# Kernel tuning notes

Hardware: AMD Instinct MI355X
Metric: run time of the kernel (lower is better)

Reference implementation:

```python
import jax, jax.numpy as jnp
import numpy as np

G = 8          # deformable groups
K = 9          # 3x3 kernel points
MAXR = 10.0    # max_residue_magnitude


def conv2d(x, w, b):
    # x: [B,Cin,H,W], w: [Cout,Cin,3,3], SAME padding, stride 1
    y = jax.lax.conv_general_dilated(x, w, (1, 1), ((1, 1), (1, 1)),
                                     dimension_numbers=('NCHW', 'OIHW', 'NCHW'))
    return y + b[None, :, None, None]


def lrelu(x):
    return jnp.where(x >= 0, x, 0.1 * x)


def offset_branch(x, ws, bs):
    for w, b in zip(ws[:-1], bs[:-1]):
        x = lrelu(conv2d(x, w, b))
    return conv2d(x, ws[-1], bs[-1])


def mdcn(x, offset, mask, w, b):
    # Modulated deformable conv, 3x3, stride 1, pad 1, dilation 1, groups=1.
    # offset: [B, G*K*2, H, W] ordered (g, k, (y,x)); mask: [B, G*K, H, W]
    B, C, H, W = x.shape
    Cg = C // G
    off = offset.reshape(B, G, K, 2, H, W)
    m = mask.reshape(B, G, K, H, W)
    ky = (jnp.arange(K) // 3 - 1).astype(x.dtype)   # kernel dy, pad=1
    kx = (jnp.arange(K) % 3 - 1).astype(x.dtype)    # kernel dx
    hy = jnp.arange(H, dtype=x.dtype)
    wx = jnp.arange(W, dtype=x.dtype)
    py = hy[None, None, None, :, None] + ky[None, None, :, None, None] + off[:, :, :, 0]  # [B,G,K,H,W]
    px = wx[None, None, None, None, :] + kx[None, None, :, None, None] + off[:, :, :, 1]
    y0f = jnp.floor(py); x0f = jnp.floor(px)
    ly = py - y0f; lx = px - x0f
    y0 = y0f.astype(jnp.int32); x0 = x0f.astype(jnp.int32)
    xf = x.reshape(B, G, Cg, H * W)

    def gather(yi, xi):
        valid = ((yi >= 0) & (yi < H) & (xi >= 0) & (xi < W)).astype(x.dtype)
        yc = jnp.clip(yi, 0, H - 1)
        xc = jnp.clip(xi, 0, W - 1)
        idx = (yc * W + xc).reshape(B, G, 1, K * H * W)
        v = jnp.take_along_axis(xf, idx, axis=3).reshape(B, G, Cg, K, H, W)
        return v * valid.reshape(B, G, 1, K, H, W)

    ly_ = ly[:, :, None]; lx_ = lx[:, :, None]  # [B,G,1,K,H,W]
    samp = (gather(y0, x0) * (1 - ly_) * (1 - lx_)
            + gather(y0, x0 + 1) * (1 - ly_) * lx_
            + gather(y0 + 1, x0) * ly_ * (1 - lx_)
            + gather(y0 + 1, x0 + 1) * ly_ * lx_)
    samp = samp * m[:, :, None]                 # modulation
    wr = w.reshape(w.shape[0], G, Cg, K)        # [Cout,G,Cg,K]
    return jnp.einsum('ogck,bgckhw->bohw', wr, samp) + b[None, :, None, None]


def setup_inputs():
    key = jax.random.key(0)
    ks = jax.random.split(key, 40)
    B, C, H, W = 1, 64, 256, 256
    s = 0.05
    inp = {
        'feat_prev': jax.random.normal(ks[0], (B, C, H, W), jnp.float32),
        'feat_next': jax.random.normal(ks[1], (B, C, H, W), jnp.float32),
        'extra_feat_prev': jax.random.normal(ks[2], (B, 2 * C, H, W), jnp.float32),
        'extra_feat_next': jax.random.normal(ks[3], (B, 2 * C, H, W), jnp.float32),
        'flow_prev': jax.random.normal(ks[4], (B, 2, H, W), jnp.float32),
        'flow_next': jax.random.normal(ks[5], (B, 2, H, W), jnp.float32),
    }
    shapes = [(C, 2 * C, 3, 3), (C, C, 3, 3), (C, C, 3, 3), (27 * G, C, 3, 3)]
    i = 6
    for pre in ('off1', 'off2'):
        for j, sh in enumerate(shapes):
            inp[f'{pre}_w{j}'] = jax.random.normal(ks[i], sh, jnp.float32) * s; i += 1
            inp[f'{pre}_b{j}'] = jax.random.normal(ks[i], (sh[0],), jnp.float32) * s; i += 1
    inp['dcn1_w'] = jax.random.normal(ks[i], (C, C, 3, 3), jnp.float32) * s; i += 1
    inp['dcn1_b'] = jax.random.normal(ks[i], (C,), jnp.float32) * s; i += 1
    inp['dcn2_w'] = jax.random.normal(ks[i], (C, C, 3, 3), jnp.float32) * s; i += 1
    inp['dcn2_b'] = jax.random.normal(ks[i], (C,), jnp.float32) * s; i += 1
    inp['fus_w'] = jax.random.normal(ks[i], (C, 2 * C, 3, 3), jnp.float32) * s; i += 1
    inp['fus_b'] = jax.random.normal(ks[i], (C,), jnp.float32) * s
    return inp


def reference(feat_prev, feat_next, extra_feat_prev, extra_feat_next, flow_prev, flow_next,
              off1_w0, off1_b0, off1_w1, off1_b1, off1_w2, off1_b2, off1_w3, off1_b3,
              off2_w0, off2_b0, off2_w1, off2_b1, off2_w2, off2_b2, off2_w3, off2_b3,
              dcn1_w, dcn1_b, dcn2_w, dcn2_b, fus_w, fus_b):
    def branch(feat, extra, flow, ws, bs, dw, db):
        out = offset_branch(extra, ws, bs)
        o1, o2, msk = jnp.split(out, 3, axis=1)
        off = MAXR * jnp.tanh(jnp.concatenate([o1, o2], axis=1))
        off = off + jnp.tile(flow[:, ::-1], (1, off.shape[1] // 2, 1, 1))  # flip(1).repeat
        msk = jax.nn.sigmoid(msk)
        return mdcn(feat, off, msk, dw, db)

    fp = branch(feat_prev, extra_feat_prev, flow_prev,
                [off1_w0, off1_w1, off1_w2, off1_w3], [off1_b0, off1_b1, off1_b2, off1_b3],
                dcn1_w, dcn1_b)
    fn = branch(feat_next, extra_feat_next, flow_next,
                [off2_w0, off2_w1, off2_w2, off2_w3], [off2_b0, off2_b1, off2_b2, off2_b3],
                dcn2_w, dcn2_b)
    return conv2d(jnp.concatenate([fp, fn], axis=1), fus_w, fus_b)
```

## Files before the change

kernel.cpp:

```cpp
#include <hip/hip_runtime.h>
#include <cstddef>
#include <cstdint>

constexpr int IMG = 256;
constexpr int NPIX = 65536;
constexpr int PW = 258;
constexpr size_t PREC = (size_t)PW * PW;

typedef _Float16 h8 __attribute__((ext_vector_type(8)));
typedef float f32x4 __attribute__((ext_vector_type(4)));

template<int CIN>
__device__ __forceinline__ void zero_pad_rec(int i, _Float16* buf)
{
  constexpr int Q = CIN / 8;
  if (i >= 1028 * Q) return;
  int pr = i / Q, qi = i - pr * Q;
  int rec;
  if (pr < 258) rec = pr;
  else if (pr < 516) rec = 257 * 258 + (pr - 258);
  else { int j = pr - 516; rec = (1 + (j >> 1)) * 258 + ((j & 1) ? 257 : 0); }
  *reinterpret_cast<uint4*>(&buf[(size_t)rec * CIN + qi * 8]) = uint4{0, 0, 0, 0};
}

template<int CIN>
__global__ __launch_bounds__(256) void zeropad_k(_Float16* __restrict__ buf)
{
  zero_pad_rec<CIN>(blockIdx.x * 256 + threadIdx.x, buf);
}

template<int CIN>
__global__ __launch_bounds__(256) void prep_hwc_k(
    const float* __restrict__ in0, const float* __restrict__ in1,
    _Float16* __restrict__ out0, _Float16* __restrict__ out1)
{
  const int z = blockIdx.z;
  const float* in = z ? in1 : in0;
  _Float16* out = z ? out1 : out0;
  int b = blockIdx.x;
  if (b >= 256) { zero_pad_rec<CIN>((b - 256) * 256 + threadIdx.x, out); return; }
  int pix = b * 256 + threadIdx.x;
  int py = pix >> 8, px = pix & 255;
  size_t rec = ((size_t)(py + 1) * PW + px + 1) * CIN;
#pragma unroll
  for (int c0 = 0; c0 < CIN; c0 += 8) {
    _Float16 t[8];
#pragma unroll
    for (int j = 0; j < 8; ++j)
      t[j] = (_Float16)in[(size_t)(c0 + j) * NPIX + pix];
    *reinterpret_cast<uint4*>(&out[rec + c0]) = *reinterpret_cast<uint4*>(t);
  }
}

__device__ __forceinline__ void wfrag(
    const float* __restrict__ w, int cin_tot, int cin_off, int KC, int NBF,
    int nvalid, int idx, _Float16* __restrict__ oHi, _Float16* __restrict__ oLo)
{
  int l = idx & 63;
  int r = idx >> 6;
  int fg = r % NBF; r /= NBF;
  int c = r % KC;
  int t = r / KC;
  int n = fg * 16 + (l & 15);
  int cinb = c * 32 + (l >> 4) * 8;
  _Float16 vh[8], vl[8];
#pragma unroll
  for (int j = 0; j < 8; ++j) {
    float x = 0.f;
    if (n < nvalid) x = w[((size_t)n * cin_tot + cin_off + cinb + j) * 9 + t];
    vh[j] = (_Float16)x;
    vl[j] = (_Float16)(x - (float)vh[j]);
  }
  *reinterpret_cast<uint4*>(oHi + (size_t)idx * 8) = *reinterpret_cast<uint4*>(vh);
  if (oLo)
    *reinterpret_cast<uint4*>(oLo + (size_t)idx * 8) = *reinterpret_cast<uint4*>(vl);
}

__global__ __launch_bounds__(256) void wprep_all_k(
    const float* __restrict__ w0, const float* __restrict__ w1,
    const float* __restrict__ w2, const float* __restrict__ w3,
    const float* __restrict__ wf, const float* __restrict__ dw,
    _Float16* b0h, _Float16* b0l, _Float16* b1h, _Float16* b1l,
    _Float16* b2h, _Float16* b2l, _Float16* b3h, _Float16* b3l,
    _Float16* bfh, _Float16* __restrict__ wB)
{
  int idx = blockIdx.x * 256 + threadIdx.x;
  if (idx < 9216)       wfrag(w0, 128, 0, 4, 4, 64, idx, b0h, b0l);
  else if (idx < 13824) wfrag(w1, 64, 0, 2, 4, 64, idx - 9216, b1h, b1l);
  else if (idx < 18432) wfrag(w2, 64, 0, 2, 4, 64, idx - 13824, b2h, b2l);
  else if (idx < 36864) wfrag(w3, 64, 0, 2, 16, 216, idx - 18432, b3h, b3l);
  else if (idx < 41472) {
    int i = idx - 36864;
    int l = i & 63;
    int r = i >> 6;
    int f = r & 3;
    int p = r >> 2;
    int t = p * 4 + (l >> 4);
    int g = (t * 57) >> 9;
    int k = t - 9 * g;
    int n = f * 16 + (l & 15);
    _Float16 v[8];
#pragma unroll
    for (int j = 0; j < 8; ++j)
      v[j] = (_Float16)dw[(size_t)n * 576 + g * 72 + j * 9 + k];
    *reinterpret_cast<uint4*>(wB + (size_t)i * 8) = *reinterpret_cast<uint4*>(v);
  }
  else if (wf && idx < 50688)
    wfrag(wf, 128, 0, 4, 4, 64, idx - 41472, bfh, nullptr);
}

template<int CIN, int EPI, bool DBL, typename OT>
__global__ __launch_bounds__(256) void conv_mfma_k(
    const _Float16* __restrict__ act0, const _Float16* __restrict__ act1,
    const _Float16* __restrict__ wHi0, const _Float16* __restrict__ wHi1,
    const _Float16* __restrict__ wLo0, const _Float16* __restrict__ wLo1,
    const float* __restrict__ bias0, const float* __restrict__ bias1,
    OT* __restrict__ out0, OT* __restrict__ out1, int ncout, int NBF)
{
  constexpr int Q = CIN / 8;
  constexpr int KC = CIN / 32;
  constexpr int NT = DBL ? 2 : 1;
  constexpr int NREC = 198;
  __shared__ __align__(16) _Float16 sA[NREC * CIN];

  const int z = blockIdx.z;
  const _Float16* __restrict__ act = z ? act1 : act0;
  const _Float16* __restrict__ wHi = z ? wHi1 : wHi0;
  const _Float16* __restrict__ wLo = z ? wLo1 : wLo0;
  const float* __restrict__ bias = z ? bias1 : bias0;
  OT* __restrict__ out = z ? out1 : out0;

  const int tid = threadIdx.x;
  const int lane = tid & 63;
  const int wv = tid >> 6;
  const int b = blockIdx.x;
  const int inner = b >> 3;
  const int y = (b & 7) * 32 + (inner & 31);
  const int x0 = (inner >> 5) << 6;
  const int n0 = blockIdx.y << 6;

  for (int i = tid; i < NREC * Q; i += 256) {
    int rec = i / Q, q = i - rec * Q;
    int seg = rec / 66, xr = rec - seg * 66;
    size_t g = ((size_t)(y + seg) * PW + x0 + xr) * CIN + q * 8;
    int slot = (q + rec) & (Q - 1);
    *reinterpret_cast<uint4*>(&sA[rec * CIN + slot * 8]) =
        *reinterpret_cast<const uint4*>(&act[g]);
  }

  const int fgb = (n0 >> 4) + wv;
  auto bload = [&](int t, int c, const _Float16* src) {
    return *reinterpret_cast<const h8*>(
        &src[((((size_t)t * KC + c) * NBF + fgb) * 64 + lane) * 8]);
  };
  h8 Bn[KC][NT];
#pragma unroll
  for (int c = 0; c < KC; ++c) {
    Bn[c][0] = bload(0, c, wHi);
    if (DBL) Bn[c][1] = bload(0, c, wLo);
  }

  f32x4 acc[4];
#pragma unroll
  for (int a = 0; a < 4; ++a) acc[a] = f32x4{0.f, 0.f, 0.f, 0.f};
  __syncthreads();

  const int m = lane & 15, kq = lane >> 4;
#pragma unroll 1
  for (int t = 0; t < 9; ++t) {
    h8 Bc[KC][NT];
#pragma unroll
    for (int c = 0; c < KC; ++c) {
      Bc[c][0] = Bn[c][0];
      if (DBL) Bc[c][1] = Bn[c][1];
    }
    if (t < 8) {
#pragma unroll
      for (int c = 0; c < KC; ++c) {
        Bn[c][0] = bload(t + 1, c, wHi);
        if (DBL) Bn[c][1] = bload(t + 1, c, wLo);
      }
    }
    const int lrb = (t / 3) * 66 + (t % 3) + m;
#pragma unroll
    for (int c = 0; c < KC; ++c) {
      const int q = c * 4 + kq;
#pragma unroll
      for (int mf = 0; mf < 4; ++mf) {
        int lr = lrb + mf * 16;
        int slot = (q + lr) & (Q - 1);
        h8 ah = *reinterpret_cast<const h8*>(&sA[lr * CIN + slot * 8]);
        acc[mf] = __builtin_amdgcn_mfma_f32_16x16x32_f16(
            ah, Bc[c][0], acc[mf], 0, 0, 0);
        if (DBL)
          acc[mf] = __builtin_amdgcn_mfma_f32_16x16x32_f16(
              ah, Bc[c][1], acc[mf], 0, 0, 0);
      }
    }
  }

  if (EPI == 0) {
    const int ch = wv * 16 + m;
    const float bv = bias[ch];
#pragma unroll
    for (int mf = 0; mf < 4; ++mf)
#pragma unroll
      for (int r = 0; r < 4; ++r) {
        int p = mf * 16 + kq * 4 + r;
        float v = acc[mf][r] + bv;
        v = (v >= 0.f) ? v : 0.1f * v;
        reinterpret_cast<_Float16*>(out)[((size_t)(y + 1) * PW + x0 + p + 1) * 64 + ch] =
            (_Float16)v;
      }
  } else {
    __syncthreads();
    float* sF = reinterpret_cast<float*>(sA);
    const int nl = wv * 16 + m;
#pragma unroll
    for (int mf = 0; mf < 4; ++mf) {
      int ml = mf * 16 + kq * 4;
      f32x4 v = acc[mf];
      float bv = (n0 + nl < ncout) ? bias[n0 + nl] : 0.f;
      v[0] += bv; v[1] += bv; v[2] += bv; v[3] += bv;
      *reinterpret_cast<f32x4*>(&sF[nl * 68 + ml]) = v;
    }
    __syncthreads();
    for (int i = tid; i < 1024; i += 256) {
      int row = i >> 4, cx = (i & 15) * 4;
      int gc = n0 + row;
      if (gc < ncout) {
        f32x4 v = *reinterpret_cast<f32x4*>(&sF[row * 68 + cx]);
        size_t ob = (size_t)gc * NPIX + (size_t)y * IMG + x0 + cx;
        if (sizeof(OT) == 2) {
          _Float16 t4[4] = {(_Float16)v[0], (_Float16)v[1],
                            (_Float16)v[2], (_Float16)v[3]};
          *reinterpret_cast<uint2*>(reinterpret_cast<_Float16*>(out) + ob) =
              *reinterpret_cast<uint2*>(t4);
        } else {
          *reinterpret_cast<f32x4*>(reinterpret_cast<float*>(out) + ob) = v;
        }
      }
    }
  }
}

__global__ __launch_bounds__(256) void featg_k(
    const float* __restrict__ in0, const float* __restrict__ in1,
    _Float16* __restrict__ out0, _Float16* __restrict__ out1)
{
  const int z = blockIdx.z;
  const float* in = z ? in1 : in0;
  _Float16* out = z ? out1 : out0;
  int pix = blockIdx.x * 256 + threadIdx.x;
#pragma unroll
  for (int g = 0; g < 8; ++g) {
    _Float16 t[8];
#pragma unroll
    for (int c = 0; c < 8; ++c)
      t[c] = (_Float16)in[(size_t)(g * 8 + c) * NPIX + pix];
    *reinterpret_cast<uint4*>(&out[((size_t)g * NPIX + pix) * 8]) =
        *reinterpret_cast<uint4*>(t);
  }
}

struct GS {
  h8 a, b, c, d;
  _Float16 w00, w01, w10, w11;
  float r0, r1, r2;
};

__global__ __launch_bounds__(256, 4) void mdcn_mfma_k(
    const _Float16* __restrict__ featG0, const _Float16* __restrict__ featG1,
    const _Float16* __restrict__ o2160, const _Float16* __restrict__ o2161,
    const float* __restrict__ flow0, const float* __restrict__ flow1,
    const _Float16* __restrict__ wB0, const _Float16* __restrict__ wB1,
    const float* __restrict__ bias0, const float* __restrict__ bias1,
    _Float16* __restrict__ actF)
{
  __shared__ __align__(16) _Float16 sWB[3 * 2048];

  const int z = blockIdx.z;
  const char* __restrict__ featGc =
      reinterpret_cast<const char*>(z ? featG1 : featG0);
  const char* __restrict__ o216c =
      reinterpret_cast<const char*>(z ? o2161 : o2160);
  const float* __restrict__ flow = z ? flow1 : flow0;
  const char* __restrict__ wBc = reinterpret_cast<const char*>(z ? wB1 : wB0);
  const float* __restrict__ bias = z ? bias1 : bias0;
  const int zoff = z << 6;

  const int tid = threadIdx.x;
  const int lane = tid & 63;
  const int wv = tid >> 6;
  const int b = blockIdx.x;
  const int inner = b >> 3;
  const int row = (b & 7) * 32 + (inner & 31);
  const int xseg = inner >> 5;
  const int m = lane & 15;
  const int tq = lane >> 4;
  const int xw = xseg * 64 + wv * 16;
  const int x = xw + m;
  const int pix = row * 256 + x;

  const float fy = flow[NPIX + pix];
  const float fx = flow[pix];
  const float rowf = (float)row, xf = (float)x;
  const uint32_t wvb = (uint32_t)wv << 10;
  const uint32_t lane16 = (uint32_t)lane * 16;
  const int wvh = wv << 9;

  f32x4 acc[4];
#pragma unroll
  for (int f = 0; f < 4; ++f) acc[f] = f32x4{0.f, 0.f, 0.f, 0.f};

  uint32_t ro0 = ((uint32_t)(2 * tq) * NPIX + (uint32_t)pix) * 2;
  uint32_t ro2 = ((uint32_t)(144 + tq) * NPIX + (uint32_t)pix) * 2;
  auto rawloadv = [&](float& a0, float& a1, float& a2) {
    a0 = (float)*reinterpret_cast<const _Float16*>(o216c + ro0);
    a1 = (float)*reinterpret_cast<const _Float16*>(o216c + ro0 + NPIX * 2);
    a2 = (float)*reinterpret_cast<const _Float16*>(o216c + ro2);
    ro0 += 8u * NPIX * 2;
    ro2 += 4u * NPIX * 2;
  };

  auto setup = [&](int p, float s0, float s1, float s2, GS& o) {
    const int t = p * 4 + tq;
    const int g = (t * 57) >> 9;
    const int k = t - 9 * g;
    const int kd = (k * 11) >> 5;
    const int km = k - 3 * kd;
    const float mm = __builtin_amdgcn_rcpf(1.f + __expf(-s2));
    const float e0 = __expf(2.f * s0);
    const float e1 = __expf(2.f * s1);
    const float th0 = 1.f - 2.f * __builtin_amdgcn_rcpf(e0 + 1.f);
    const float th1 = 1.f - 2.f * __builtin_amdgcn_rcpf(e1 + 1.f);
    const float pyf = rowf + (float)(kd - 1) + 10.f * th0 + fy;
    const float pxf = xf + (float)(km - 1) + 10.f * th1 + fx;
    const float y0f = floorf(pyf), x0f = floorf(pxf);
    const float ly = pyf - y0f, lx = pxf - x0f;
    const int y0 = (int)y0f, x0i = (int)x0f;
    const int y1 = y0 + 1, x1 = x0i + 1;
    const bool vy0 = (unsigned)y0 < (unsigned)IMG, vy1 = (unsigned)y1 < (unsigned)IMG;
    const bool vx0 = (unsigned)x0i < (unsigned)IMG, vx1 = (unsigned)x1 < (unsigned)IMG;
    const int y0c = min(max(y0, 0), IMG - 1), y1c = min(max(y1, 0), IMG - 1);
    const int x0c = min(max(x0i, 0), IMG - 1), x1c = min(max(x1, 0), IMG - 1);
    const float oy = 1.f - ly, ox = 1.f - lx;
    const float py0 = oy * mm, py1 = ly * mm;
    const float w00 = (vy0 && vx0) ? py0 * ox : 0.f;
    const float w01 = (vy0 && vx1) ? py0 * lx : 0.f;
    const float w10 = (vy1 && vx0) ? py1 * ox : 0.f;
    const float w11 = (vy1 && vx1) ? py1 * lx : 0.f;
    o.w00 = (_Float16)w00; o.w01 = (_Float16)w01;
    o.w10 = (_Float16)w10; o.w11 = (_Float16)w11;
    const uint32_t gb = ((uint32_t)g << 16);
    const uint32_t ry0 = gb + ((uint32_t)y0c << 8);
    const uint32_t ry1 = gb + ((uint32_t)y1c << 8);
    o.a = *reinterpret_cast<const h8*>(featGc + ((ry0 + x0c) << 4));
    o.b = *reinterpret_cast<const h8*>(featGc + ((ry0 + x1c) << 4));
    o.c = *reinterpret_cast<const h8*>(featGc + ((ry1 + x0c) << 4));
    o.d = *reinterpret_cast<const h8*>(featGc + ((ry1 + x1c) << 4));
  };

  auto consume = [&](GS& cur, int bufi) {
    const _Float16* wp = &sWB[bufi * 2048 + lane * 8];
    h8 bf0 = *reinterpret_cast<const h8*>(wp);
    h8 bf1 = *reinterpret_cast<const h8*>(wp + 512);
    h8 bf2 = *reinterpret_cast<const h8*>(wp + 1024);
    h8 bf3 = *reinterpret_cast<const h8*>(wp + 1536);
    h8 af = cur.a * cur.w00 + cur.b * cur.w01 +
            cur.c * cur.w10 + cur.d * cur.w11;
    acc[0] = __builtin_amdgcn_mfma_f32_16x16x32_f16(af, bf0, acc[0], 0, 0, 0);
    acc[1] = __builtin_amdgcn_mfma_f32_16x16x32_f16(af, bf1, acc[1], 0, 0, 0);
    acc[2] = __builtin_amdgcn_mfma_f32_16x16x32_f16(af, bf2, acc[2], 0, 0, 0);
    acc[3] = __builtin_amdgcn_mfma_f32_16x16x32_f16(af, bf3, acc[3], 0, 0, 0);
  };

  auto body = [&](int p, int bc, GS& cur, GS& nxt) {
    const int bs = (bc == 2) ? 0 : bc + 1;
    h8 tw = *reinterpret_cast<const h8*>(
        wBc + (size_t)(p + 1) * 4096 + wvb + lane16);
    rawloadv(cur.r0, cur.r1, cur.r2);
    *reinterpret_cast<h8*>(&sWB[bs * 2048 + wvh + lane * 8]) = tw;
    __syncthreads();
    setup(p + 1, nxt.r0, nxt.r1, nxt.r2, nxt);
    consume(cur, bc);
  };

  GS A, B;
  {
    h8 tw = *reinterpret_cast<const h8*>(wBc + wvb + lane16);
    float t0, t1, t2;
    rawloadv(t0, t1, t2);
    rawloadv(B.r0, B.r1, B.r2);
    *reinterpret_cast<h8*>(&sWB[wvh + lane * 8]) = tw;
    setup(0, t0, t1, t2, A);
  }

  int bc = 0;
#pragma unroll 1
  for (int it = 0; it < 8; ++it) {
    body(2 * it, bc, A, B);
    bc = (bc == 2) ? 0 : bc + 1;
    body(2 * it + 1, bc, B, A);
    bc = (bc == 2) ? 0 : bc + 1;
  }
  {
    h8 tw = *reinterpret_cast<const h8*>(
        wBc + (size_t)17 * 4096 + wvb + lane16);
    setup(17, B.r0, B.r1, B.r2, B);
    *reinterpret_cast<h8*>(&sWB[2 * 2048 + wvh + lane * 8]) = tw;
    __syncthreads();
    consume(A, 1);
    consume(B, 2);
  }

  const size_t rb = ((size_t)(row + 1) * PW + xw + 1) * 128 + zoff;
#pragma unroll
  for (int f = 0; f < 4; ++f) {
    const int ch = f * 16 + m;
    const float bv = bias[ch];
#pragma unroll
    for (int r = 0; r < 4; ++r)
      actF[rb + (size_t)(tq * 4 + r) * 128 + ch] = (_Float16)(acc[f][r] + bv);
  }
}

extern "C" void kernel_launch(void* const* d_in, const int* in_sizes, int n_in,
                              void* d_out, int out_size, void* d_ws, size_t ws_size,
                              hipStream_t stream)
{
  const float* feat[2]  = {(const float*)d_in[0], (const float*)d_in[1]};
  const float* extra[2] = {(const float*)d_in[2], (const float*)d_in[3]};
  const float* flow[2]  = {(const float*)d_in[4], (const float*)d_in[5]};
  const float* ow[2][4];
  const float* ob[2][4];
  for (int br = 0; br < 2; ++br)
    for (int j = 0; j < 4; ++j) {
      ow[br][j] = (const float*)d_in[6 + br * 8 + j * 2];
      ob[br][j] = (const float*)d_in[6 + br * 8 + j * 2 + 1];
    }
  const float* dcnw[2] = {(const float*)d_in[22], (const float*)d_in[24]};
  const float* dcnb[2] = {(const float*)d_in[23], (const float*)d_in[25]};
  const float* fusw = (const float*)d_in[26];
  const float* fusb = (const float*)d_in[27];

  char* wsb = (char*)d_ws;
  size_t off = 0;
  auto alloc = [&](size_t bytes) {
    void* p = wsb + off;
    off += (bytes + 255) & ~(size_t)255;
    return p;
  };
  _Float16* R1 = (_Float16*)alloc(PREC * 128 * 2 * 2);
  _Float16* actI0 = R1;
  _Float16* actI1 = R1 + PREC * 128;
  _Float16* actB0 = R1;
  _Float16* actB1 = R1 + PREC * 64;
  _Float16* actF  = R1;
  _Float16* R2 = (_Float16*)alloc(PREC * 64 * 2 * 2);
  _Float16* actA0 = R2;
  _Float16* actA1 = R2 + PREC * 64;
  _Float16* featG0 = R2;
  _Float16* featG1 = R2 + PREC * 64;
  _Float16* o2160 = (_Float16*)alloc((size_t)216 * NPIX * 2 * 2);
  _Float16* o2161 = o2160 + (size_t)216 * NPIX;
  _Float16* wB0 = (_Float16*)alloc(73728 * 2);
  _Float16* wB1 = wB0 + 36864;
  _Float16* wb0h[2] = {(_Float16*)alloc(147456), (_Float16*)alloc(147456)};
  _Float16* wb0l[2] = {(_Float16*)alloc(147456), (_Float16*)alloc(147456)};
  _Float16* wb1h[2] = {(_Float16*)alloc(73728), (_Float16*)alloc(73728)};
  _Float16* wb1l[2] = {(_Float16*)alloc(73728), (_Float16*)alloc(73728)};
  _Float16* wb2h[2] = {(_Float16*)alloc(73728), (_Float16*)alloc(73728)};
  _Float16* wb2l[2] = {(_Float16*)alloc(73728), (_Float16*)alloc(73728)};
  _Float16* wb3h[2] = {(_Float16*)alloc(294912), (_Float16*)alloc(294912)};
  _Float16* wb3l[2] = {(_Float16*)alloc(294912), (_Float16*)alloc(294912)};
  _Float16* wbFh = (_Float16*)alloc(147456);
  float* outp = (float*)d_out;

  dim3 blk256(256);
  zeropad_k<64><<<dim3(33), blk256, 0, stream>>>(actA0);
  zeropad_k<64><<<dim3(33), blk256, 0, stream>>>(actA1);

  wprep_all_k<<<dim3(198), blk256, 0, stream>>>(
      ow[0][0], ow[0][1], ow[0][2], ow[0][3], fusw, dcnw[0],
      wb0h[0], wb0l[0], wb1h[0], wb1l[0], wb2h[0], wb2l[0],
      wb3h[0], wb3l[0], wbFh, wB0);
  wprep_all_k<<<dim3(162), blk256, 0, stream>>>(
      ow[1][0], ow[1][1], ow[1][2], ow[1][3], nullptr, dcnw[1],
      wb0h[1], wb0l[1], wb1h[1], wb1l[1], wb2h[1], wb2l[1],
      wb3h[1], wb3l[1], nullptr, wB1);

  prep_hwc_k<128><<<dim3(321, 1, 2), blk256, 0, stream>>>(
      extra[0], extra[1], actI0, actI1);

  conv_mfma_k<128, 0, true, _Float16><<<dim3(1024, 1, 2), blk256, 0, stream>>>(
      actI0, actI1, wb0h[0], wb0h[1], wb0l[0], wb0l[1],
      ob[0][0], ob[1][0], actA0, actA1, 64, 4);
  zeropad_k<64><<<dim3(33), blk256, 0, stream>>>(actB0);
  zeropad_k<64><<<dim3(33), blk256, 0, stream>>>(actB1);
  conv_mfma_k<64, 0, true, _Float16><<<dim3(1024, 1, 2), blk256, 0, stream>>>(
      actA0, actA1, wb1h[0], wb1h[1], wb1l[0], wb1l[1],
      ob[0][1], ob[1][1], actB0, actB1, 64, 4);
  conv_mfma_k<64, 0, true, _Float16><<<dim3(1024, 1, 2), blk256, 0, stream>>>(
      actB0, actB1, wb2h[0], wb2h[1], wb2l[0], wb2l[1],
      ob[0][2], ob[1][2], actA0, actA1, 64, 4);
  zeropad_k<128><<<dim3(65), blk256, 0, stream>>>(actF);
  conv_mfma_k<64, 1, true, _Float16><<<dim3(1024, 4, 2), blk256, 0, stream>>>(
      actA0, actA1, wb3h[0], wb3h[1], wb3l[0], wb3l[1],
      ob[0][3], ob[1][3], o2160, o2161, 216, 16);

  featg_k<<<dim3(256, 1, 2), blk256, 0, stream>>>(
      feat[0], feat[1], featG0, featG1);
  mdcn_mfma_k<<<dim3(1024, 1, 2), blk256, 0, stream>>>(
      featG0, featG1, o2160, o2161, flow[0], flow[1],
      wB0, wB1, dcnb[0], dcnb[1], actF);

  conv_mfma_k<128, 1, false, float><<<dim3(1024, 1, 1), blk256, 0, stream>>>(
      actF, actF, wbFh, wbFh, nullptr, nullptr,
      fusb, fusb, outp, outp, 64, 4);
}
```

Baseline: 488.4 us.

## Split MDCN reduction over two phases and sum partials in fusion conv load

The deformable conv kernel's 18-step reduction over group/kernel-point tiles is split into two halves along a new grid dimension. Each half writes its partial sum to its own padded buffer, with bias added only by the first half. The fusion conv gains a SUM2 mode that adds the two partial buffers while staging activations into shared memory. The aim is to double the parallelism of the MDCN launch and raise occupancy, at the cost of an extra padded buffer, an extra zero-pad launch, doubled reads in the final conv, and an fp16 rounding of each partial before summation.

```diff
diff --git a/kernel.cpp b/kernel.cpp
--- a/kernel.cpp
+++ b/kernel.cpp
@@ -109,9 +109,10 @@
     wfrag(wf, 128, 0, 4, 4, 64, idx - 41472, bfh, nullptr);
 }
 
-template<int CIN, int EPI, bool DBL, typename OT>
+template<int CIN, int EPI, bool DBL, bool SUM2, typename OT>
 __global__ __launch_bounds__(256) void conv_mfma_k(
     const _Float16* __restrict__ act0, const _Float16* __restrict__ act1,
+    const _Float16* __restrict__ act20, const _Float16* __restrict__ act21,
     const _Float16* __restrict__ wHi0, const _Float16* __restrict__ wHi1,
     const _Float16* __restrict__ wLo0, const _Float16* __restrict__ wLo1,
     const float* __restrict__ bias0, const float* __restrict__ bias1,
@@ -125,6 +126,7 @@
 
   const int z = blockIdx.z;
   const _Float16* __restrict__ act = z ? act1 : act0;
+  const _Float16* __restrict__ act2 = z ? act21 : act20;
   const _Float16* __restrict__ wHi = z ? wHi1 : wHi0;
   const _Float16* __restrict__ wLo = z ? wLo1 : wLo0;
   const float* __restrict__ bias = z ? bias1 : bias0;
@@ -144,8 +146,16 @@
     int seg = rec / 66, xr = rec - seg * 66;
     size_t g = ((size_t)(y + seg) * PW + x0 + xr) * CIN + q * 8;
     int slot = (q + rec) & (Q - 1);
-    *reinterpret_cast<uint4*>(&sA[rec * CIN + slot * 8]) =
-        *reinterpret_cast<const uint4*>(&act[g]);
+    if (SUM2) {
+      h8 va = *reinterpret_cast<const h8*>(&act[g]);
+      h8 vb = *reinterpret_cast<const h8*>(&act2[g]);
+      h8 s = va + vb;
+      *reinterpret_cast<uint4*>(&sA[rec * CIN + slot * 8]) =
+          *reinterpret_cast<uint4*>(&s);
+    } else {
+      *reinterpret_cast<uint4*>(&sA[rec * CIN + slot * 8]) =
+          *reinterpret_cast<const uint4*>(&act[g]);
+    }
   }
 
   const int fgb = (n0 >> 4) + wv;
@@ -275,11 +285,13 @@
     const float* __restrict__ flow0, const float* __restrict__ flow1,
     const _Float16* __restrict__ wB0, const _Float16* __restrict__ wB1,
     const float* __restrict__ bias0, const float* __restrict__ bias1,
-    _Float16* __restrict__ actF)
+    _Float16* __restrict__ actF0, _Float16* __restrict__ actF1)
 {
   __shared__ __align__(16) _Float16 sWB[3 * 2048];
 
   const int z = blockIdx.z;
+  const int ph = blockIdx.y;
+  const int pbase = ph * 9;
   const char* __restrict__ featGc =
       reinterpret_cast<const char*>(z ? featG1 : featG0);
   const char* __restrict__ o216c =
@@ -287,6 +299,7 @@
   const float* __restrict__ flow = z ? flow1 : flow0;
   const char* __restrict__ wBc = reinterpret_cast<const char*>(z ? wB1 : wB0);
   const float* __restrict__ bias = z ? bias1 : bias0;
+  _Float16* __restrict__ actFp = ph ? actF1 : actF0;
   const int zoff = z << 6;
 
   const int tid = threadIdx.x;
@@ -313,8 +326,8 @@
 #pragma unroll
   for (int f = 0; f < 4; ++f) acc[f] = f32x4{0.f, 0.f, 0.f, 0.f};
 
-  uint32_t ro0 = ((uint32_t)(2 * tq) * NPIX + (uint32_t)pix) * 2;
-  uint32_t ro2 = ((uint32_t)(144 + tq) * NPIX + (uint32_t)pix) * 2;
+  uint32_t ro0 = ((uint32_t)(8 * pbase + 2 * tq) * NPIX + (uint32_t)pix) * 2;
+  uint32_t ro2 = ((uint32_t)(144 + 4 * pbase + tq) * NPIX + (uint32_t)pix) * 2;
   auto rawloadv = [&](float& a0, float& a1, float& a2) {
     a0 = (float)*reinterpret_cast<const _Float16*>(o216c + ro0);
     a1 = (float)*reinterpret_cast<const _Float16*>(o216c + ro0 + NPIX * 2);
@@ -388,40 +401,45 @@
 
   GS A, B;
   {
-    h8 tw = *reinterpret_cast<const h8*>(wBc + wvb + lane16);
+    h8 tw = *reinterpret_cast<const h8*>(
+        wBc + (size_t)pbase * 4096 + wvb + lane16);
     float t0, t1, t2;
     rawloadv(t0, t1, t2);
     rawloadv(B.r0, B.r1, B.r2);
     *reinterpret_cast<h8*>(&sWB[wvh + lane * 8]) = tw;
-    setup(0, t0, t1, t2, A);
+    setup(pbase, t0, t1, t2, A);
   }
 
   int bc = 0;
 #pragma unroll 1
-  for (int it = 0; it < 8; ++it) {
-    body(2 * it, bc, A, B);
+  for (int it = 0; it < 3; ++it) {
+    body(pbase + 2 * it, bc, A, B);
     bc = (bc == 2) ? 0 : bc + 1;
-    body(2 * it + 1, bc, B, A);
+    body(pbase + 2 * it + 1, bc, B, A);
     bc = (bc == 2) ? 0 : bc + 1;
   }
+  body(pbase + 6, bc, A, B);
+  bc = (bc == 2) ? 0 : bc + 1;
   {
+    const int bs = (bc == 2) ? 0 : bc + 1;
     h8 tw = *reinterpret_cast<const h8*>(
-        wBc + (size_t)17 * 4096 + wvb + lane16);
-    setup(17, B.r0, B.r1, B.r2, B);
-    *reinterpret_cast<h8*>(&sWB[2 * 2048 + wvh + lane * 8]) = tw;
+        wBc + (size_t)(pbase + 8) * 4096 + wvb + lane16);
+    *reinterpret_cast<h8*>(&sWB[bs * 2048 + wvh + lane * 8]) = tw;
     __syncthreads();
-    consume(A, 1);
-    consume(B, 2);
-  }
+    setup(pbase + 8, A.r0, A.r1, A.r2, A);
+    consume(B, bc);
+    bc = bs;
+  }
+  consume(A, bc);
 
   const size_t rb = ((size_t)(row + 1) * PW + xw + 1) * 128 + zoff;
 #pragma unroll
   for (int f = 0; f < 4; ++f) {
     const int ch = f * 16 + m;
-    const float bv = bias[ch];
+    const float bv = ph ? 0.f : bias[ch];
 #pragma unroll
     for (int r = 0; r < 4; ++r)
-      actF[rb + (size_t)(tq * 4 + r) * 128 + ch] = (_Float16)(acc[f][r] + bv);
+      actFp[rb + (size_t)(tq * 4 + r) * 128 + ch] = (_Float16)(acc[f][r] + bv);
   }
 }
 
@@ -456,7 +474,8 @@
   _Float16* actI1 = R1 + PREC * 128;
   _Float16* actB0 = R1;
   _Float16* actB1 = R1 + PREC * 64;
-  _Float16* actF  = R1;
+  _Float16* actF0 = R1;
+  _Float16* actF1 = R1 + PREC * 128;
   _Float16* R2 = (_Float16*)alloc(PREC * 64 * 2 * 2);
   _Float16* actA0 = R2;
   _Float16* actA1 = R2 + PREC * 64;
@@ -493,29 +512,30 @@
   prep_hwc_k<128><<<dim3(321, 1, 2), blk256, 0, stream>>>(
       extra[0], extra[1], actI0, actI1);
 
-  conv_mfma_k<128, 0, true, _Float16><<<dim3(1024, 1, 2), blk256, 0, stream>>>(
-      actI0, actI1, wb0h[0], wb0h[1], wb0l[0], wb0l[1],
+  conv_mfma_k<128, 0, true, false, _Float16><<<dim3(1024, 1, 2), blk256, 0, stream>>>(
+      actI0, actI1, nullptr, nullptr, wb0h[0], wb0h[1], wb0l[0], wb0l[1],
       ob[0][0], ob[1][0], actA0, actA1, 64, 4);
   zeropad_k<64><<<dim3(33), blk256, 0, stream>>>(actB0);
   zeropad_k<64><<<dim3(33), blk256, 0, stream>>>(actB1);
-  conv_mfma_k<64, 0, true, _Float16><<<dim3(1024, 1, 2), blk256, 0, stream>>>(
-      actA0, actA1, wb1h[0], wb1h[1], wb1l[0], wb1l[1],
+  conv_mfma_k<64, 0, true, false, _Float16><<<dim3(1024, 1, 2), blk256, 0, stream>>>(
+      actA0, actA1, nullptr, nullptr, wb1h[0], wb1h[1], wb1l[0], wb1l[1],
       ob[0][1], ob[1][1], actB0, actB1, 64, 4);
-  conv_mfma_k<64, 0, true, _Float16><<<dim3(1024, 1, 2), blk256, 0, stream>>>(
-      actB0, actB1, wb2h[0], wb2h[1], wb2l[0], wb2l[1],
+  conv_mfma_k<64, 0, true, false, _Float16><<<dim3(1024, 1, 2), blk256, 0, stream>>>(
+      actB0, actB1, nullptr, nullptr, wb2h[0], wb2h[1], wb2l[0], wb2l[1],
       ob[0][2], ob[1][2], actA0, actA1, 64, 4);
-  zeropad_k<128><<<dim3(65), blk256, 0, stream>>>(actF);
-  conv_mfma_k<64, 1, true, _Float16><<<dim3(1024, 4, 2), blk256, 0, stream>>>(
-      actA0, actA1, wb3h[0], wb3h[1], wb3l[0], wb3l[1],
+  zeropad_k<128><<<dim3(65), blk256, 0, stream>>>(actF0);
+  zeropad_k<128><<<dim3(65), blk256, 0, stream>>>(actF1);
+  conv_mfma_k<64, 1, true, false, _Float16><<<dim3(1024, 4, 2), blk256, 0, stream>>>(
+      actA0, actA1, nullptr, nullptr, wb3h[0], wb3h[1], wb3l[0], wb3l[1],
       ob[0][3], ob[1][3], o2160, o2161, 216, 16);
 
   featg_k<<<dim3(256, 1, 2), blk256, 0, stream>>>(
       feat[0], feat[1], featG0, featG1);
-  mdcn_mfma_k<<<dim3(1024, 1, 2), blk256, 0, stream>>>(
+  mdcn_mfma_k<<<dim3(1024, 2, 2), blk256, 0, stream>>>(
       featG0, featG1, o2160, o2161, flow[0], flow[1],
-      wB0, wB1, dcnb[0], dcnb[1], actF);
-
-  conv_mfma_k<128, 1, false, float><<<dim3(1024, 1, 1), blk256, 0, stream>>>(
-      actF, actF, wbFh, wbFh, nullptr, nullptr,
+      wB0, wB1, dcnb[0], dcnb[1], actF0, actF1);
+
+  conv_mfma_k<128, 1, false, true, float><<<dim3(1024, 1, 1), blk256, 0, stream>>>(
+      actF0, actF0, actF1, actF1, wbFh, wbFh, nullptr, nullptr,
       fusb, fusb, outp, outp, 64, 4);
 }
```

Result: slower. 509.7 us (+4.4%).
